# Kernel optimization log

Measured on AMD Instinct MI355X. Metric: run time of the kernel, lower is better.

Reference implementation:

```python
import jax, jax.numpy as jnp
import numpy as np

B, S, D, H = 2, 2048, 768, 12
DK = D // H
NEG = -1e9

def setup_inputs() -> dict:
    key = jax.random.key(0)
    ks = jax.random.split(key, 12)
    def lin(k):
        kw, kb = jax.random.split(k)
        lim = 1.0 / np.sqrt(D)
        W = jax.random.uniform(kw, (D, D), jnp.float32, -lim, lim)
        b = jax.random.uniform(kb, (D,), jnp.float32, -lim, lim)
        return W, b
    Wq, bq = lin(ks[0]); Wk, bk = lin(ks[1]); Wv, bv = lin(ks[2]); Wo, bo = lin(ks[3])
    query = jax.random.normal(ks[4], (B, S, D), jnp.float32)
    key_t = jax.random.normal(ks[5], (B, S, D), jnp.float32)
    value = jax.random.normal(ks[6], (B, S, D), jnp.float32)
    mask = jax.random.randint(ks[7], (B, S, S), 0, 2, jnp.int32)
    return {"query": query, "key": key_t, "value": value, "mask": mask,
            "Wq": Wq, "bq": bq, "Wk": Wk, "bk": bk, "Wv": Wv, "bv": bv,
            "Wo": Wo, "bo": bo}

def reference(query, key, value, mask, Wq, bq, Wk, bk, Wv, bv, Wo, bo):
    # project and split heads: [B,S,D] -> [B,H,S,DK]
    def proj(x, W, b):
        return (x @ W.T + b).reshape(B, S, H, DK).transpose(0, 2, 1, 3)
    q = proj(query, Wq, bq)
    k = proj(key, Wk, bk)
    v = proj(value, Wv, bv)
    scale = np.float32(1.0 / np.sqrt(DK))
    scores = jnp.einsum('bhqd,bhkd->bhqk', q, k) * scale  # [B,H,S,S]
    scores = jnp.where(mask[:, None, :, :] == 0, jnp.float32(NEG), scores)
    log_attn = jax.nn.log_softmax(scores, axis=-1)  # [B,H,S,S]
    p_attn = jnp.exp(log_attn)                      # softmax, shares reduction
    x = jnp.einsum('bhqk,bhkd->bhqd', p_attn, v)    # [B,H,S,DK]
    x = x.transpose(0, 2, 1, 3).reshape(B, S, D)
    out = x @ Wo.T + bo
    return out, log_attn
```

## Files before the change

### kernel.cpp

```cpp
#include <hip/hip_runtime.h>

#define B_ 2
#define S_ 2048
#define D_ 768
#define H_ 12
#define DK_ 64
#define BH_ (B_*H_)
#define NEGV (-1e9f)
#define SCALE 0.125f
#define MINIT (-1e30f)

typedef unsigned short u16;
typedef __attribute__((ext_vector_type(8))) short bf16x8;
typedef __attribute__((ext_vector_type(4))) float f32x4;

__device__ __forceinline__ float bf2f(u16 u){
  union { unsigned int i; float f; } v; v.i = ((unsigned int)u) << 16; return v.f;
}
__device__ __forceinline__ u16 f2bf(float f){
  union { float f; unsigned int i; } v; v.f = f;
  unsigned int x = v.i;
  return (u16)((x + 0x7FFFu + ((x >> 16) & 1u)) >> 16);
}
__device__ __forceinline__ void split2(float x, u16& h, u16& l){
  const unsigned int xi = __float_as_uint(x);
  h = (u16)(xi >> 16);
  const float lo = x - __uint_as_float(xi & 0xFFFF0000u);
  l = (u16)(__float_as_uint(lo) >> 16);
}

template<bool XBF16, int OMODE>
__device__ __forceinline__ void gemmM(const void* __restrict__ Xp_, const float* __restrict__ W,
                                      const float* __restrict__ bias, void* __restrict__ outp)
{
  const int bx = blockIdx.x, by = blockIdx.y;
  const int tid  = threadIdx.x;
  const int lane = tid & 63;
  const int w    = tid >> 6;
  const int g    = lane >> 4;
  const int c    = lane & 15;
  const int wr   = w >> 1, wc = w & 1;

  __shared__ u16 Ah[128][36];
  __shared__ u16 Al[128][36];
  __shared__ u16 Bh[128][36];
  __shared__ u16 Bl[128][36];

  const int ar0 = (OMODE==2 ? by : bx) * 128;
  const int br0 = (OMODE==2 ? bx : by) * 128;

  const float* __restrict__ Afp = (OMODE==2) ? W : (const float*)Xp_;
  const float* __restrict__ Bfp = (OMODE==2) ? (const float*)Xp_ : W;
  const u16*   __restrict__ Abp = (const u16*)Xp_;

  f32x4 acc[4][4];
  #pragma unroll
  for (int m=0;m<4;m++)
    #pragma unroll
    for (int n=0;n<4;n++) acc[m][n] = (f32x4){0.f,0.f,0.f,0.f};

  for (int k0 = 0; k0 < D_; k0 += 32) {
    __syncthreads();
    if constexpr (XBF16) {
      #pragma unroll
      for (int i=0;i<2;i++){
        const int ci = tid + i*256;
        const int row = ci >> 2, c8 = (ci & 3) * 8;
        *(uint4*)&Ah[row][c8] = *(const uint4*)(Abp + (size_t)(ar0+row)*D_ + k0 + c8);
      }
    } else {
      #pragma unroll
      for (int i=0;i<4;i++){
        const int ci = tid + i*256;
        const int row = ci >> 3, c4 = (ci & 7) * 4;
        float4 v = *(const float4*)(Afp + (size_t)(ar0+row)*D_ + k0 + c4);
        ushort4 hv, lv;
        split2(v.x,hv.x,lv.x); split2(v.y,hv.y,lv.y); split2(v.z,hv.z,lv.z); split2(v.w,hv.w,lv.w);
        *(ushort4*)&Ah[row][c4] = hv;
        *(ushort4*)&Al[row][c4] = lv;
      }
    }
    #pragma unroll
    for (int i=0;i<4;i++){
      const int ci = tid + i*256;
      const int row = ci >> 3, c4 = (ci & 7) * 4;
      float4 v = *(const float4*)(Bfp + (size_t)(br0+row)*D_ + k0 + c4);
      ushort4 hv, lv;
      split2(v.x,hv.x,lv.x); split2(v.y,hv.y,lv.y); split2(v.z,hv.z,lv.z); split2(v.w,hv.w,lv.w);
      *(ushort4*)&Bh[row][c4] = hv;
      *(ushort4*)&Bl[row][c4] = lv;
    }
    __syncthreads();

    bf16x8 ah[4], al[4], bh[4], bl[4];
    #pragma unroll
    for (int m=0;m<4;m++){
      ah[m] = *(const bf16x8*)&Ah[wr*64 + m*16 + c][g*8];
      if constexpr (!XBF16) al[m] = *(const bf16x8*)&Al[wr*64 + m*16 + c][g*8];
    }
    #pragma unroll
    for (int n=0;n<4;n++){
      bh[n] = *(const bf16x8*)&Bh[wc*64 + n*16 + c][g*8];
      bl[n] = *(const bf16x8*)&Bl[wc*64 + n*16 + c][g*8];
    }
    #pragma unroll
    for (int m=0;m<4;m++)
      #pragma unroll
      for (int n=0;n<4;n++){
        acc[m][n] = __builtin_amdgcn_mfma_f32_16x16x32_bf16(ah[m], bh[n], acc[m][n], 0,0,0);
        acc[m][n] = __builtin_amdgcn_mfma_f32_16x16x32_bf16(ah[m], bl[n], acc[m][n], 0,0,0);
        if constexpr (!XBF16)
          acc[m][n] = __builtin_amdgcn_mfma_f32_16x16x32_bf16(al[m], bh[n], acc[m][n], 0,0,0);
      }
  }

  if constexpr (OMODE==0) {
    float* out = (float*)outp;
    float bb[4];
    #pragma unroll
    for (int n=0;n<4;n++) bb[n] = bias[br0 + wc*64 + n*16 + c];
    #pragma unroll
    for (int m=0;m<4;m++)
      #pragma unroll
      for (int r=0;r<4;r++){
        const int rg = ar0 + wr*64 + m*16 + g*4 + r;
        #pragma unroll
        for (int n=0;n<4;n++)
          out[(size_t)rg*D_ + br0 + wc*64 + n*16 + c] = acc[m][n][r] + bb[n];
      }
  } else if constexpr (OMODE==1) {
    u16* out = (u16*)outp;
    float bb[4];
    #pragma unroll
    for (int n=0;n<4;n++) bb[n] = bias[br0 + wc*64 + n*16 + c];
    #pragma unroll
    for (int m=0;m<4;m++)
      #pragma unroll
      for (int r=0;r<4;r++){
        const int rg = ar0 + wr*64 + m*16 + g*4 + r;
        const int batch = rg >> 11, s = rg & (S_-1);
        #pragma unroll
        for (int n=0;n<4;n++){
          const int col = br0 + wc*64 + n*16 + c;
          const int hh = col >> 6, dk = col & 63;
          out[((size_t)(batch*H_ + hh)*S_ + s)*DK_ + dk] = f2bf(acc[m][n][r] + bb[n]);
        }
      }
  } else {
    u16* out = (u16*)outp;
    #pragma unroll
    for (int m=0;m<4;m++)
      #pragma unroll
      for (int r=0;r<4;r++){
        const int dkg = ar0 + wr*64 + m*16 + g*4 + r;
        const int hh = dkg >> 6, dkl = dkg & 63;
        const float bb = bias[dkg];
        #pragma unroll
        for (int n=0;n<4;n++){
          const int sg = br0 + wc*64 + n*16 + c;
          const int batch = sg >> 11, s = sg & (S_-1);
          out[((size_t)(batch*H_ + hh)*DK_ + dkl)*S_ + s] = f2bf(acc[m][n][r] + bb);
        }
      }
  }
}

__global__ __launch_bounds__(256) void proj_qkv(
    const float* __restrict__ Xq, const float* __restrict__ Xk, const float* __restrict__ Xv,
    const float* __restrict__ Wq, const float* __restrict__ bq,
    const float* __restrict__ Wk, const float* __restrict__ bk,
    const float* __restrict__ Wv, const float* __restrict__ bv,
    u16* __restrict__ qkv)
{
  const int z = blockIdx.z;
  u16* out = qkv + (size_t)z * ((size_t)BH_*S_*DK_);
  if (z==0)      gemmM<false,1>((const void*)Xq, Wq, bq, (void*)out);
  else if (z==1) gemmM<false,1>((const void*)Xk, Wk, bk, (void*)out);
  else           gemmM<false,2>((const void*)Xv, Wv, bv, (void*)out);
}

__global__ __launch_bounds__(256) void proj_o(
    const u16* __restrict__ Xc, const float* __restrict__ Wo, const float* __restrict__ bo,
    float* __restrict__ out)
{
  gemmM<true,0>((const void*)Xc, Wo, bo, (void*)out);
}

__device__ __forceinline__ void stage64(u16 (*dst)[72], const u16* __restrict__ src,
                                        size_t sstride, int tid)
{
  #pragma unroll
  for (int i=0;i<2;i++){
    const int cidx = tid + i*256;
    const int row = cidx >> 3, cc = (cidx & 7) << 3;
    uint4 v = *(const uint4*)(src + (size_t)row*sstride + cc);
    *(uint4*)&dst[row][cc] = v;
  }
}

__global__ __launch_bounds__(256,3) void attn(const u16* __restrict__ qkv, const int* __restrict__ mask,
                                              float* __restrict__ la, u16* __restrict__ ctx)
{
  const int bh = blockIdx.y;
  const int q0 = blockIdx.x * 64;
  const int b = bh / H_;
  const int h = bh - b*H_;
  const u16* Qp = qkv + (size_t)bh * S_ * DK_;
  const u16* Kp = qkv + (size_t)(BH_ + bh) * S_ * DK_;
  const u16* Vt = qkv + (size_t)(2*BH_ + bh) * S_ * DK_;
  const int* Mp = mask + (size_t)b * S_ * S_;

  const int tid  = threadIdx.x;
  const int w    = tid >> 6;
  const int lane = tid & 63;
  const int g    = lane >> 4;
  const int c    = lane & 15;

  __shared__ u16 Ks[64][72];
  __shared__ u16 Vs[64][72];
  __shared__ u16 Ps[4][16][72];

  stage64(Ks, Qp + (size_t)q0*DK_, DK_, tid);
  __syncthreads();
  const bf16x8 qf0 = *(const bf16x8*)&Ks[w*16 + c][g*8];
  const bf16x8 qf1 = *(const bf16x8*)&Ks[w*16 + c][g*8 + 32];

  float mt[4], lt[4];
  #pragma unroll
  for (int r=0;r<4;r++){ mt[r] = MINIT; lt[r] = 0.f; }

  for (int j0=0; j0<S_; j0+=64){
    __syncthreads();
    stage64(Ks, Kp + (size_t)j0*DK_, DK_, tid);
    __syncthreads();
    f32x4 sc[4];
    #pragma unroll
    for (int nt=0; nt<4; nt++){
      const bf16x8 kf0 = *(const bf16x8*)&Ks[nt*16 + c][g*8];
      const bf16x8 kf1 = *(const bf16x8*)&Ks[nt*16 + c][g*8 + 32];
      f32x4 z = {0.f,0.f,0.f,0.f};
      z      = __builtin_amdgcn_mfma_f32_16x16x32_bf16(qf0, kf0, z, 0,0,0);
      sc[nt] = __builtin_amdgcn_mfma_f32_16x16x32_bf16(qf1, kf1, z, 0,0,0);
    }
    #pragma unroll
    for (int r=0;r<4;r++){
      const int qi = q0 + w*16 + g*4 + r;
      const int* mp = Mp + (size_t)qi*S_ + j0 + c;
      float sv[4];
      #pragma unroll
      for (int nt=0;nt<4;nt++)
        sv[nt] = mp[nt*16] ? sc[nt][r]*SCALE : NEGV;
      const float cm = fmaxf(fmaxf(sv[0],sv[1]), fmaxf(sv[2],sv[3]));
      const float mn = fmaxf(mt[r], cm);
      lt[r] = lt[r]*__expf(mt[r]-mn)
            + __expf(sv[0]-mn) + __expf(sv[1]-mn) + __expf(sv[2]-mn) + __expf(sv[3]-mn);
      mt[r] = mn;
    }
  }

  float ml[4];
  #pragma unroll
  for (int r=0;r<4;r++){
    float m = mt[r], l = lt[r];
    #pragma unroll
    for (int st=1; st<16; st<<=1){
      const float m2 = __shfl_xor(m, st);
      const float l2 = __shfl_xor(l, st);
      const float mn = fmaxf(m, m2);
      l = l*__expf(m-mn) + l2*__expf(m2-mn);
      m = mn;
    }
    ml[r] = m + __logf(fmaxf(l, 1e-30f));
  }

  f32x4 o[4];
  #pragma unroll
  for (int nt=0;nt<4;nt++) o[nt] = (f32x4){0.f,0.f,0.f,0.f};

  for (int j0=0; j0<S_; j0+=64){
    __syncthreads();
    stage64(Ks, Kp + (size_t)j0*DK_, DK_, tid);
    stage64(Vs, Vt + j0, S_, tid);
    __syncthreads();
    f32x4 sc[4];
    #pragma unroll
    for (int nt=0; nt<4; nt++){
      const bf16x8 kf0 = *(const bf16x8*)&Ks[nt*16 + c][g*8];
      const bf16x8 kf1 = *(const bf16x8*)&Ks[nt*16 + c][g*8 + 32];
      f32x4 z = {0.f,0.f,0.f,0.f};
      z      = __builtin_amdgcn_mfma_f32_16x16x32_bf16(qf0, kf0, z, 0,0,0);
      sc[nt] = __builtin_amdgcn_mfma_f32_16x16x32_bf16(qf1, kf1, z, 0,0,0);
    }
    float lvv[4][4];
    #pragma unroll
    for (int r=0;r<4;r++){
      const int qi = q0 + w*16 + g*4 + r;
      const int* mp = Mp + (size_t)qi*S_ + j0 + c;
      #pragma unroll
      for (int nt=0;nt<4;nt++){
        const float s  = mp[nt*16] ? sc[nt][r]*SCALE : NEGV;
        const float lv = fminf(s - ml[r], 0.f);
        lvv[r][nt] = lv;
        Ps[w][g*4+r][nt*16 + c] = f2bf(__expf(lv));
      }
    }
    __syncthreads();
    const bf16x8 pf0 = *(const bf16x8*)&Ps[w][c][g*8];
    const bf16x8 pf1 = *(const bf16x8*)&Ps[w][c][g*8 + 32];
    #pragma unroll
    for (int nt=0; nt<4; nt++){
      const bf16x8 vf0 = *(const bf16x8*)&Vs[nt*16 + c][g*8];
      const bf16x8 vf1 = *(const bf16x8*)&Vs[nt*16 + c][g*8 + 32];
      o[nt] = __builtin_amdgcn_mfma_f32_16x16x32_bf16(pf0, vf0, o[nt], 0,0,0);
      o[nt] = __builtin_amdgcn_mfma_f32_16x16x32_bf16(pf1, vf1, o[nt], 0,0,0);
    }
    #pragma unroll
    for (int r=0;r<4;r++){
      const int qi = q0 + w*16 + g*4 + r;
      float* lrow = la + ((size_t)bh*S_ + qi)*S_ + j0 + c;
      #pragma unroll
      for (int nt=0;nt<4;nt++) lrow[nt*16] = lvv[r][nt];
    }
  }

  #pragma unroll
  for (int r=0;r<4;r++){
    const int qi = q0 + w*16 + g*4 + r;
    u16* crow = ctx + ((size_t)b*S_ + qi)*D_ + h*DK_ + c;
    #pragma unroll
    for (int nt=0;nt<4;nt++) crow[nt*16] = f2bf(o[nt][r]);
  }
}

extern "C" void kernel_launch(void* const* d_in, const int* in_sizes, int n_in,
                              void* d_out, int out_size, void* d_ws, size_t ws_size,
                              hipStream_t stream)
{
  const float* query = (const float*)d_in[0];
  const float* key   = (const float*)d_in[1];
  const float* value = (const float*)d_in[2];
  const int* mask    = (const int*)d_in[3];
  const float* Wq = (const float*)d_in[4];  const float* bq = (const float*)d_in[5];
  const float* Wk = (const float*)d_in[6];  const float* bk = (const float*)d_in[7];
  const float* Wv = (const float*)d_in[8];  const float* bv = (const float*)d_in[9];
  const float* Wo = (const float*)d_in[10]; const float* bo = (const float*)d_in[11];

  float* out = (float*)d_out;
  float* la  = out + (size_t)B_*S_*D_;
  u16* qkvws = (u16*)d_ws;
  u16* ctx = qkvws + (size_t)3*BH_*S_*DK_;

  proj_qkv<<<dim3(32,6,3), dim3(256,1,1), 0, stream>>>(query,key,value,Wq,bq,Wk,bk,Wv,bv,qkvws);
  attn<<<dim3(S_/64, BH_,1), dim3(256,1,1), 0, stream>>>(qkvws, mask, la, ctx);
  proj_o<<<dim3(32,6,1), dim3(256,1,1), 0, stream>>>(ctx, Wo, bo, out);
}
```

Measured before the change: 707.6 us.

## Pre-split fp32 inputs to bf16 planes, register-prefetch GEMM tiles, double-buffer attention K/V

Adds a prep kernel that splits X and W for the Q/K/V projections into bf16 hi/lo planes once, written into the log_attn output buffer as scratch, so the projection GEMM no longer re-splits each tile. The GEMM and both attention passes now prefetch the next tile into registers while the current one is computed, and attention uses double-buffered LDS for K/V, which removes one barrier per iteration. The softmax statistics pass skips the rescale when no lane's row max grows. The cost is an extra kernel launch, an extra write and read of the split data, and higher register and LDS pressure.

```diff
diff --git a/kernel.cpp b/kernel.cpp
--- a/kernel.cpp
+++ b/kernel.cpp
@@ -14,9 +14,6 @@
 typedef __attribute__((ext_vector_type(8))) short bf16x8;
 typedef __attribute__((ext_vector_type(4))) float f32x4;
 
-__device__ __forceinline__ float bf2f(u16 u){
-  union { unsigned int i; float f; } v; v.i = ((unsigned int)u) << 16; return v.f;
-}
 __device__ __forceinline__ u16 f2bf(float f){
   union { float f; unsigned int i; } v; v.f = f;
   unsigned int x = v.i;
@@ -29,8 +26,37 @@
   l = (u16)(__float_as_uint(lo) >> 16);
 }
 
-template<bool XBF16, int OMODE>
-__device__ __forceinline__ void gemmM(const void* __restrict__ Xp_, const float* __restrict__ W,
+#define XN_ ((size_t)4096*768)
+#define WN_ ((size_t)768*768)
+
+__global__ __launch_bounds__(256) void prep(
+    const float* __restrict__ Xq, const float* __restrict__ Xk, const float* __restrict__ Xv,
+    const float* __restrict__ Wq, const float* __restrict__ Wk, const float* __restrict__ Wv,
+    u16* __restrict__ scr)
+{
+  const int a = blockIdx.y;
+  const float* src; u16* h; u16* l; size_t n;
+  if (a < 3){
+    src = (a==0)?Xq:(a==1)?Xk:Xv;
+    h = scr + (size_t)a*XN_;  l = scr + (size_t)(3+a)*XN_;  n = XN_;
+  } else {
+    const int z = a-3;
+    src = (z==0)?Wq:(z==1)?Wk:Wv;
+    h = scr + 6*XN_ + (size_t)z*WN_;  l = scr + 6*XN_ + 3*WN_ + (size_t)z*WN_;  n = WN_;
+  }
+  const size_t nv = n >> 2;
+  for (size_t i = (size_t)blockIdx.x*256 + threadIdx.x; i < nv; i += (size_t)gridDim.x*256){
+    float4 v = ((const float4*)src)[i];
+    ushort4 hv, lv;
+    split2(v.x,hv.x,lv.x); split2(v.y,hv.y,lv.y); split2(v.z,hv.z,lv.z); split2(v.w,hv.w,lv.w);
+    ((ushort4*)h)[i] = hv;  ((ushort4*)l)[i] = lv;
+  }
+}
+
+template<bool ALO, bool BPRE, int OMODE>
+__device__ __forceinline__ void gemmM(const u16* __restrict__ Ah_, const u16* __restrict__ Al_,
+                                      const u16* __restrict__ Bh_, const u16* __restrict__ Bl_,
+                                      const float* __restrict__ Bf_,
                                       const float* __restrict__ bias, void* __restrict__ outp)
 {
   const int bx = blockIdx.x, by = blockIdx.y;
@@ -49,46 +75,65 @@
   const int ar0 = (OMODE==2 ? by : bx) * 128;
   const int br0 = (OMODE==2 ? bx : by) * 128;
 
-  const float* __restrict__ Afp = (OMODE==2) ? W : (const float*)Xp_;
-  const float* __restrict__ Bfp = (OMODE==2) ? (const float*)Xp_ : W;
-  const u16*   __restrict__ Abp = (const u16*)Xp_;
-
-  f32x4 acc[4][4];
-  #pragma unroll
-  for (int m=0;m<4;m++)
-    #pragma unroll
-    for (int n=0;n<4;n++) acc[m][n] = (f32x4){0.f,0.f,0.f,0.f};
-
-  for (int k0 = 0; k0 < D_; k0 += 32) {
-    __syncthreads();
-    if constexpr (XBF16) {
-      #pragma unroll
-      for (int i=0;i<2;i++){
-        const int ci = tid + i*256;
-        const int row = ci >> 2, c8 = (ci & 3) * 8;
-        *(uint4*)&Ah[row][c8] = *(const uint4*)(Abp + (size_t)(ar0+row)*D_ + k0 + c8);
-      }
-    } else {
-      #pragma unroll
-      for (int i=0;i<4;i++){
-        const int ci = tid + i*256;
-        const int row = ci >> 3, c4 = (ci & 7) * 4;
-        float4 v = *(const float4*)(Afp + (size_t)(ar0+row)*D_ + k0 + c4);
-        ushort4 hv, lv;
-        split2(v.x,hv.x,lv.x); split2(v.y,hv.y,lv.y); split2(v.z,hv.z,lv.z); split2(v.w,hv.w,lv.w);
-        *(ushort4*)&Ah[row][c4] = hv;
-        *(ushort4*)&Al[row][c4] = lv;
-      }
-    }
+  uint4 rah[2], ral[2], rbh[2], rbl[2];
+  float4 rbf[4];
+
+  auto ldplane = [&](uint4* r, const u16* base, int rbase, int k0){
+    #pragma unroll
+    for (int i=0;i<2;i++){
+      const int ci = tid + i*256;
+      const int row = ci >> 2, c8 = (ci & 3)*8;
+      r[i] = *(const uint4*)(base + (size_t)(rbase+row)*D_ + k0 + c8);
+    }
+  };
+  auto stplane = [&](u16 (*P)[36], const uint4* r){
+    #pragma unroll
+    for (int i=0;i<2;i++){
+      const int ci = tid + i*256;
+      const int row = ci >> 2, c8 = (ci & 3)*8;
+      *(uint4*)&P[row][c8] = r[i];
+    }
+  };
+  auto ldBf = [&](int k0){
     #pragma unroll
     for (int i=0;i<4;i++){
       const int ci = tid + i*256;
-      const int row = ci >> 3, c4 = (ci & 7) * 4;
-      float4 v = *(const float4*)(Bfp + (size_t)(br0+row)*D_ + k0 + c4);
+      const int row = ci >> 3, c4 = (ci & 7)*4;
+      rbf[i] = *(const float4*)(Bf_ + (size_t)(br0+row)*D_ + k0 + c4);
+    }
+  };
+  auto stBf = [&](){
+    #pragma unroll
+    for (int i=0;i<4;i++){
+      const int ci = tid + i*256;
+      const int row = ci >> 3, c4 = (ci & 7)*4;
       ushort4 hv, lv;
-      split2(v.x,hv.x,lv.x); split2(v.y,hv.y,lv.y); split2(v.z,hv.z,lv.z); split2(v.w,hv.w,lv.w);
-      *(ushort4*)&Bh[row][c4] = hv;
-      *(ushort4*)&Bl[row][c4] = lv;
+      split2(rbf[i].x,hv.x,lv.x); split2(rbf[i].y,hv.y,lv.y);
+      split2(rbf[i].z,hv.z,lv.z); split2(rbf[i].w,hv.w,lv.w);
+      *(ushort4*)&Bh[row][c4] = hv;  *(ushort4*)&Bl[row][c4] = lv;
+    }
+  };
+
+  f32x4 acc[4][4];
+  #pragma unroll
+  for (int m=0;m<4;m++)
+    #pragma unroll
+    for (int n=0;n<4;n++) acc[m][n] = (f32x4){0.f,0.f,0.f,0.f};
+
+  ldplane(rah, Ah_, ar0, 0);
+  if constexpr (ALO) ldplane(ral, Al_, ar0, 0);
+  if constexpr (BPRE){ ldplane(rbh, Bh_, br0, 0); ldplane(rbl, Bl_, br0, 0); } else ldBf(0);
+
+  for (int t=0; t<D_/32; ++t){
+    __syncthreads();
+    stplane(Ah, rah);
+    if constexpr (ALO) stplane(Al, ral);
+    if constexpr (BPRE){ stplane(Bh, rbh); stplane(Bl, rbl); } else stBf();
+    if (t < D_/32 - 1){
+      const int k0n = (t+1)*32;
+      ldplane(rah, Ah_, ar0, k0n);
+      if constexpr (ALO) ldplane(ral, Al_, ar0, k0n);
+      if constexpr (BPRE){ ldplane(rbh, Bh_, br0, k0n); ldplane(rbl, Bl_, br0, k0n); } else ldBf(k0n);
     }
     __syncthreads();
 
@@ -96,7 +141,7 @@
     #pragma unroll
     for (int m=0;m<4;m++){
       ah[m] = *(const bf16x8*)&Ah[wr*64 + m*16 + c][g*8];
-      if constexpr (!XBF16) al[m] = *(const bf16x8*)&Al[wr*64 + m*16 + c][g*8];
+      if constexpr (ALO) al[m] = *(const bf16x8*)&Al[wr*64 + m*16 + c][g*8];
     }
     #pragma unroll
     for (int n=0;n<4;n++){
@@ -109,7 +154,7 @@
       for (int n=0;n<4;n++){
         acc[m][n] = __builtin_amdgcn_mfma_f32_16x16x32_bf16(ah[m], bh[n], acc[m][n], 0,0,0);
         acc[m][n] = __builtin_amdgcn_mfma_f32_16x16x32_bf16(ah[m], bl[n], acc[m][n], 0,0,0);
-        if constexpr (!XBF16)
+        if constexpr (ALO)
           acc[m][n] = __builtin_amdgcn_mfma_f32_16x16x32_bf16(al[m], bh[n], acc[m][n], 0,0,0);
       }
   }
@@ -165,36 +210,43 @@
   }
 }
 
-__global__ __launch_bounds__(256) void proj_qkv(
-    const float* __restrict__ Xq, const float* __restrict__ Xk, const float* __restrict__ Xv,
-    const float* __restrict__ Wq, const float* __restrict__ bq,
-    const float* __restrict__ Wk, const float* __restrict__ bk,
-    const float* __restrict__ Wv, const float* __restrict__ bv,
+__global__ __launch_bounds__(256,2) void proj_qkv(
+    const u16* __restrict__ scr,
+    const float* __restrict__ bq, const float* __restrict__ bk, const float* __restrict__ bv,
     u16* __restrict__ qkv)
 {
   const int z = blockIdx.z;
   u16* out = qkv + (size_t)z * ((size_t)BH_*S_*DK_);
-  if (z==0)      gemmM<false,1>((const void*)Xq, Wq, bq, (void*)out);
-  else if (z==1) gemmM<false,1>((const void*)Xk, Wk, bk, (void*)out);
-  else           gemmM<false,2>((const void*)Xv, Wv, bv, (void*)out);
-}
-
-__global__ __launch_bounds__(256) void proj_o(
+  const u16* Xh = scr + (size_t)z*XN_;
+  const u16* Xl = scr + (size_t)(3+z)*XN_;
+  const u16* Wh = scr + 6*XN_ + (size_t)z*WN_;
+  const u16* Wl = scr + 6*XN_ + 3*WN_ + (size_t)z*WN_;
+  const float* bias = (z==0)?bq:(z==1)?bk:bv;
+  if (z==2) gemmM<true,true,2>(Wh, Wl, Xh, Xl, nullptr, bias, (void*)out);
+  else      gemmM<true,true,1>(Xh, Xl, Wh, Wl, nullptr, bias, (void*)out);
+}
+
+__global__ __launch_bounds__(256,2) void proj_o(
     const u16* __restrict__ Xc, const float* __restrict__ Wo, const float* __restrict__ bo,
     float* __restrict__ out)
 {
-  gemmM<true,0>((const void*)Xc, Wo, bo, (void*)out);
-}
-
-__device__ __forceinline__ void stage64(u16 (*dst)[72], const u16* __restrict__ src,
-                                        size_t sstride, int tid)
-{
+  gemmM<false,false,0>(Xc, nullptr, nullptr, nullptr, Wo, bo, (void*)out);
+}
+
+__device__ __forceinline__ void loadT(uint4* r, const u16* __restrict__ src, size_t sstride, int tid){
   #pragma unroll
   for (int i=0;i<2;i++){
-    const int cidx = tid + i*256;
-    const int row = cidx >> 3, cc = (cidx & 7) << 3;
-    uint4 v = *(const uint4*)(src + (size_t)row*sstride + cc);
-    *(uint4*)&dst[row][cc] = v;
+    const int ci = tid + i*256;
+    const int row = ci >> 3, cc = (ci & 7) << 3;
+    r[i] = *(const uint4*)(src + (size_t)row*sstride + cc);
+  }
+}
+__device__ __forceinline__ void writeT(u16 (*dst)[72], const uint4* r, int tid){
+  #pragma unroll
+  for (int i=0;i<2;i++){
+    const int ci = tid + i*256;
+    const int row = ci >> 3, cc = (ci & 7) << 3;
+    *(uint4*)&dst[row][cc] = r[i];
   }
 }
 
@@ -216,45 +268,58 @@
   const int g    = lane >> 4;
   const int c    = lane & 15;
 
-  __shared__ u16 Ks[64][72];
-  __shared__ u16 Vs[64][72];
+  __shared__ u16 KsB[2][64][72];
+  __shared__ u16 VsB[2][64][72];
   __shared__ u16 Ps[4][16][72];
 
-  stage64(Ks, Qp + (size_t)q0*DK_, DK_, tid);
+  {
+    uint4 qr[2];
+    loadT(qr, Qp + (size_t)q0*DK_, DK_, tid);
+    writeT(VsB[0], qr, tid);
+  }
   __syncthreads();
-  const bf16x8 qf0 = *(const bf16x8*)&Ks[w*16 + c][g*8];
-  const bf16x8 qf1 = *(const bf16x8*)&Ks[w*16 + c][g*8 + 32];
+  const bf16x8 qf0 = *(const bf16x8*)&VsB[0][w*16 + c][g*8];
+  const bf16x8 qf1 = *(const bf16x8*)&VsB[0][w*16 + c][g*8 + 32];
 
   float mt[4], lt[4];
   #pragma unroll
   for (int r=0;r<4;r++){ mt[r] = MINIT; lt[r] = 0.f; }
 
-  for (int j0=0; j0<S_; j0+=64){
-    __syncthreads();
-    stage64(Ks, Kp + (size_t)j0*DK_, DK_, tid);
-    __syncthreads();
-    f32x4 sc[4];
-    #pragma unroll
-    for (int nt=0; nt<4; nt++){
-      const bf16x8 kf0 = *(const bf16x8*)&Ks[nt*16 + c][g*8];
-      const bf16x8 kf1 = *(const bf16x8*)&Ks[nt*16 + c][g*8 + 32];
-      f32x4 z = {0.f,0.f,0.f,0.f};
-      z      = __builtin_amdgcn_mfma_f32_16x16x32_bf16(qf0, kf0, z, 0,0,0);
-      sc[nt] = __builtin_amdgcn_mfma_f32_16x16x32_bf16(qf1, kf1, z, 0,0,0);
-    }
-    #pragma unroll
-    for (int r=0;r<4;r++){
-      const int qi = q0 + w*16 + g*4 + r;
-      const int* mp = Mp + (size_t)qi*S_ + j0 + c;
-      float sv[4];
-      #pragma unroll
-      for (int nt=0;nt<4;nt++)
-        sv[nt] = mp[nt*16] ? sc[nt][r]*SCALE : NEGV;
-      const float cm = fmaxf(fmaxf(sv[0],sv[1]), fmaxf(sv[2],sv[3]));
-      const float mn = fmaxf(mt[r], cm);
-      lt[r] = lt[r]*__expf(mt[r]-mn)
-            + __expf(sv[0]-mn) + __expf(sv[1]-mn) + __expf(sv[2]-mn) + __expf(sv[3]-mn);
-      mt[r] = mn;
+  {
+    uint4 kr[2];
+    loadT(kr, Kp, DK_, tid);
+    writeT(KsB[0], kr, tid);
+    for (int t=0; t<S_/64; ++t){
+      __syncthreads();
+      if (t < S_/64-1) loadT(kr, Kp + (size_t)(t+1)*64*DK_, DK_, tid);
+      const u16 (*KT)[72] = KsB[t&1];
+      f32x4 sc[4];
+      #pragma unroll
+      for (int nt=0; nt<4; nt++){
+        const bf16x8 kf0 = *(const bf16x8*)&KT[nt*16 + c][g*8];
+        const bf16x8 kf1 = *(const bf16x8*)&KT[nt*16 + c][g*8 + 32];
+        f32x4 z = {0.f,0.f,0.f,0.f};
+        z      = __builtin_amdgcn_mfma_f32_16x16x32_bf16(qf0, kf0, z, 0,0,0);
+        sc[nt] = __builtin_amdgcn_mfma_f32_16x16x32_bf16(qf1, kf1, z, 0,0,0);
+      }
+      #pragma unroll
+      for (int r=0;r<4;r++){
+        const int qi = q0 + w*16 + g*4 + r;
+        const int* mp = Mp + (size_t)qi*S_ + (size_t)t*64 + c;
+        float sv[4];
+        #pragma unroll
+        for (int nt=0;nt<4;nt++)
+          sv[nt] = mp[nt*16] ? sc[nt][r]*SCALE : NEGV;
+        const float cm = fmaxf(fmaxf(sv[0],sv[1]), fmaxf(sv[2],sv[3]));
+        if (!__all(cm <= mt[r])){
+          const float mn = fmaxf(mt[r], cm);
+          lt[r] *= __expf(mt[r]-mn);
+          mt[r] = mn;
+        }
+        lt[r] += __expf(sv[0]-mt[r]) + __expf(sv[1]-mt[r])
+               + __expf(sv[2]-mt[r]) + __expf(sv[3]-mt[r]);
+      }
+      if (t < S_/64-1) writeT(KsB[(t+1)&1], kr, tid);
     }
   }
 
@@ -277,49 +342,62 @@
   #pragma unroll
   for (int nt=0;nt<4;nt++) o[nt] = (f32x4){0.f,0.f,0.f,0.f};
 
-  for (int j0=0; j0<S_; j0+=64){
-    __syncthreads();
-    stage64(Ks, Kp + (size_t)j0*DK_, DK_, tid);
-    stage64(Vs, Vt + j0, S_, tid);
-    __syncthreads();
-    f32x4 sc[4];
-    #pragma unroll
-    for (int nt=0; nt<4; nt++){
-      const bf16x8 kf0 = *(const bf16x8*)&Ks[nt*16 + c][g*8];
-      const bf16x8 kf1 = *(const bf16x8*)&Ks[nt*16 + c][g*8 + 32];
-      f32x4 z = {0.f,0.f,0.f,0.f};
-      z      = __builtin_amdgcn_mfma_f32_16x16x32_bf16(qf0, kf0, z, 0,0,0);
-      sc[nt] = __builtin_amdgcn_mfma_f32_16x16x32_bf16(qf1, kf1, z, 0,0,0);
-    }
-    float lvv[4][4];
-    #pragma unroll
-    for (int r=0;r<4;r++){
-      const int qi = q0 + w*16 + g*4 + r;
-      const int* mp = Mp + (size_t)qi*S_ + j0 + c;
-      #pragma unroll
-      for (int nt=0;nt<4;nt++){
-        const float s  = mp[nt*16] ? sc[nt][r]*SCALE : NEGV;
-        const float lv = fminf(s - ml[r], 0.f);
-        lvv[r][nt] = lv;
-        Ps[w][g*4+r][nt*16 + c] = f2bf(__expf(lv));
-      }
-    }
-    __syncthreads();
-    const bf16x8 pf0 = *(const bf16x8*)&Ps[w][c][g*8];
-    const bf16x8 pf1 = *(const bf16x8*)&Ps[w][c][g*8 + 32];
-    #pragma unroll
-    for (int nt=0; nt<4; nt++){
-      const bf16x8 vf0 = *(const bf16x8*)&Vs[nt*16 + c][g*8];
-      const bf16x8 vf1 = *(const bf16x8*)&Vs[nt*16 + c][g*8 + 32];
-      o[nt] = __builtin_amdgcn_mfma_f32_16x16x32_bf16(pf0, vf0, o[nt], 0,0,0);
-      o[nt] = __builtin_amdgcn_mfma_f32_16x16x32_bf16(pf1, vf1, o[nt], 0,0,0);
-    }
-    #pragma unroll
-    for (int r=0;r<4;r++){
-      const int qi = q0 + w*16 + g*4 + r;
-      float* lrow = la + ((size_t)bh*S_ + qi)*S_ + j0 + c;
-      #pragma unroll
-      for (int nt=0;nt<4;nt++) lrow[nt*16] = lvv[r][nt];
+  {
+    uint4 kr[2], vr[2];
+    loadT(kr, Kp, DK_, tid);
+    loadT(vr, Vt, S_, tid);
+    writeT(KsB[0], kr, tid);
+    writeT(VsB[0], vr, tid);
+    for (int t=0; t<S_/64; ++t){
+      __syncthreads();
+      if (t < S_/64-1){
+        loadT(kr, Kp + (size_t)(t+1)*64*DK_, DK_, tid);
+        loadT(vr, Vt + (size_t)(t+1)*64, S_, tid);
+      }
+      const u16 (*KT)[72] = KsB[t&1];
+      const u16 (*VT)[72] = VsB[t&1];
+      f32x4 sc[4];
+      #pragma unroll
+      for (int nt=0; nt<4; nt++){
+        const bf16x8 kf0 = *(const bf16x8*)&KT[nt*16 + c][g*8];
+        const bf16x8 kf1 = *(const bf16x8*)&KT[nt*16 + c][g*8 + 32];
+        f32x4 z = {0.f,0.f,0.f,0.f};
+        z      = __builtin_amdgcn_mfma_f32_16x16x32_bf16(qf0, kf0, z, 0,0,0);
+        sc[nt] = __builtin_amdgcn_mfma_f32_16x16x32_bf16(qf1, kf1, z, 0,0,0);
+      }
+      float lvv[4][4];
+      #pragma unroll
+      for (int r=0;r<4;r++){
+        const int qi = q0 + w*16 + g*4 + r;
+        const int* mp = Mp + (size_t)qi*S_ + (size_t)t*64 + c;
+        #pragma unroll
+        for (int nt=0;nt<4;nt++){
+          const float s  = mp[nt*16] ? sc[nt][r]*SCALE : NEGV;
+          const float lv = fminf(s - ml[r], 0.f);
+          lvv[r][nt] = lv;
+          Ps[w][g*4+r][nt*16 + c] = f2bf(__expf(lv));
+        }
+      }
+      const bf16x8 pf0 = *(const bf16x8*)&Ps[w][c][g*8];
+      const bf16x8 pf1 = *(const bf16x8*)&Ps[w][c][g*8 + 32];
+      #pragma unroll
+      for (int nt=0; nt<4; nt++){
+        const bf16x8 vf0 = *(const bf16x8*)&VT[nt*16 + c][g*8];
+        const bf16x8 vf1 = *(const bf16x8*)&VT[nt*16 + c][g*8 + 32];
+        o[nt] = __builtin_amdgcn_mfma_f32_16x16x32_bf16(pf0, vf0, o[nt], 0,0,0);
+        o[nt] = __builtin_amdgcn_mfma_f32_16x16x32_bf16(pf1, vf1, o[nt], 0,0,0);
+      }
+      #pragma unroll
+      for (int r=0;r<4;r++){
+        const int qi = q0 + w*16 + g*4 + r;
+        float* lrow = la + ((size_t)bh*S_ + qi)*S_ + (size_t)t*64 + c;
+        #pragma unroll
+        for (int nt=0;nt<4;nt++) lrow[nt*16] = lvv[r][nt];
+      }
+      if (t < S_/64-1){
+        writeT(KsB[(t+1)&1], kr, tid);
+        writeT(VsB[(t+1)&1], vr, tid);
+      }
     }
   }
 
@@ -349,8 +427,10 @@
   float* la  = out + (size_t)B_*S_*D_;
   u16* qkvws = (u16*)d_ws;
   u16* ctx = qkvws + (size_t)3*BH_*S_*DK_;
-
-  proj_qkv<<<dim3(32,6,3), dim3(256,1,1), 0, stream>>>(query,key,value,Wq,bq,Wk,bk,Wv,bv,qkvws);
-  attn<<<dim3(S_/64, BH_,1), dim3(256,1,1), 0, stream>>>(qkvws, mask, la, ctx);
-  proj_o<<<dim3(32,6,1), dim3(256,1,1), 0, stream>>>(ctx, Wo, bo, out);
-}
+  u16* scr = (u16*)la;
+
+  prep    <<<dim3(768,6,1),  dim3(256,1,1), 0, stream>>>(query,key,value,Wq,Wk,Wv,scr);
+  proj_qkv<<<dim3(32,6,3),   dim3(256,1,1), 0, stream>>>(scr, bq,bk,bv, qkvws);
+  attn    <<<dim3(S_/64,BH_,1), dim3(256,1,1), 0, stream>>>(qkvws, mask, la, ctx);
+  proj_o  <<<dim3(32,6,1),   dim3(256,1,1), 0, stream>>>(ctx, Wo, bo, out);
+}
```

Result: slower. 953.3 us (+34.7%).
